# Optimization experiments

Measured on AMD Instinct MI355X. Metric: run time of the kernel, lower is better.

The kernel has to match this reference:

```python
import jax, jax.numpy as jnp
import numpy as np

B, T, N, D_IN, H, K, E, L = 32, 12, 2000, 2, 64, 2, 10, 2


def setup_inputs() -> dict:
    key = jax.random.key(0)
    ks = jax.random.split(key, 2 + 4 * L)
    s = 0.05
    inp = {
        "x": jax.random.normal(ks[0], (B, T, N, D_IN), jnp.float32),
        "node_embeddings": jax.random.normal(ks[1], (N, E), jnp.float32),
    }
    dims_in = [D_IN, H]
    for l in range(L):
        din = dims_in[l] + H  # cell input is concat([x_t, state])
        inp[f"gate_w{l}"] = jax.random.normal(ks[2 + 4 * l], (E, K, din, 2 * H), jnp.float32) * s
        inp[f"gate_b{l}"] = jax.random.normal(ks[3 + 4 * l], (E, 2 * H), jnp.float32) * s
        inp[f"upd_w{l}"] = jax.random.normal(ks[4 + 4 * l], (E, K, din, H), jnp.float32) * s
        inp[f"upd_b{l}"] = jax.random.normal(ks[5 + 4 * l], (E, H), jnp.float32) * s
    return inp


def _supports(node_embeddings):
    # adaptive adjacency from node embeddings + Chebyshev-style link polynomials
    A = jax.nn.softmax(jax.nn.relu(node_embeddings @ node_embeddings.T), axis=1)  # [N,N]
    sup = [jnp.eye(N, dtype=A.dtype), A]
    for _ in range(K - 2):
        sup.append(2.0 * (A @ sup[-1]) - sup[-2])
    return jnp.stack(sup)  # [K,N,N]


def _gconv(x, supports, emb, w_pool, b_pool):
    # x: [B,N,C] -> [B,N,O]; per-node weights generated from embeddings
    W = jnp.einsum('ne,ekio->nkio', emb, w_pool)          # [N,K,C,O]
    b = emb @ b_pool                                       # [N,O]
    xg = jnp.einsum('knm,bmc->bnkc', supports, x)          # graph aggregation
    return jnp.einsum('bnki,nkio->bno', xg, W) + b


def _cell(x_t, h, supports, emb, gw, gb, uw, ub):
    xs = jnp.concatenate([x_t, h], axis=-1)
    zr = jax.nn.sigmoid(_gconv(xs, supports, emb, gw, gb))
    z, r = jnp.split(zr, 2, axis=-1)
    hc = jnp.tanh(_gconv(jnp.concatenate([x_t, z * h], axis=-1), supports, emb, uw, ub))
    return r * h + (1.0 - r) * hc


def reference(x, node_embeddings, gate_w0, gate_b0, upd_w0, upd_b0,
              gate_w1, gate_b1, upd_w1, upd_b1):
    supports = _supports(node_embeddings)
    params = [(gate_w0, gate_b0, upd_w0, upd_b0),
              (gate_w1, gate_b1, upd_w1, upd_b1)]
    cur = x
    last = None
    for gw, gb, uw, ub in params:
        h0 = jnp.zeros((x.shape[0], N, H), x.dtype)

        def step(h, x_t, gw=gw, gb=gb, uw=uw, ub=ub):
            h_new = _cell(x_t, h, supports, node_embeddings, gw, gb, uw, ub)
            return h_new, h_new

        last, outs = jax.lax.scan(step, h0, jnp.swapaxes(cur, 0, 1))
        cur = jnp.swapaxes(outs, 0, 1)  # [B,T,N,H]
    # return_all_layers=False -> last layer's full sequence output and last state
    return cur, last
```

## Files before the change

### kernel.cpp

```cpp
#include <hip/hip_runtime.h>
#include <cstdint>

#define NN 2000
#define NP 2048
#define TT 12
#define BBATCH 32
#define HH 64
#define EE 10

typedef _Float16 f16;
typedef _Float16 f16x8 __attribute__((ext_vector_type(8)));
typedef float f32x4 __attribute__((ext_vector_type(4)));
typedef unsigned int u32;

__device__ __forceinline__ void gld_lds16(const void* g, void* lds) {
    __builtin_amdgcn_global_load_lds(
        (const __attribute__((address_space(1))) u32*)(const void*)g,
        (__attribute__((address_space(3))) u32*)(void*)lds, 16, 0, 0);
}

__global__ __launch_bounds__(256) void k_supports(const float* __restrict__ emb, f16* __restrict__ A2) {
    int n = blockIdx.x;
    int tid = threadIdx.x;
    if (n >= NN) {
        for (int m = tid; m < NP; m += 256) A2[(size_t)n * NP + m] = (f16)0.f;
        return;
    }
    __shared__ float red[4];
    float en[EE];
#pragma unroll
    for (int e = 0; e < EE; e++) en[e] = emb[n * EE + e];
    float g[8];
    float mx = 0.f;
#pragma unroll
    for (int i = 0; i < 8; i++) {
        int m = tid + 256 * i;
        float v = 0.f;
        if (m < NN) {
            float a = 0.f;
#pragma unroll
            for (int e = 0; e < EE; e++) a += en[e] * emb[m * EE + e];
            v = fmaxf(a, 0.f);
            mx = fmaxf(mx, v);
        }
        g[i] = v;
    }
#pragma unroll
    for (int d = 32; d; d >>= 1) mx = fmaxf(mx, __shfl_xor(mx, d));
    if ((tid & 63) == 0) red[tid >> 6] = mx;
    __syncthreads();
    mx = fmaxf(fmaxf(red[0], red[1]), fmaxf(red[2], red[3]));
    float s = 0.f;
#pragma unroll
    for (int i = 0; i < 8; i++) {
        int m = tid + 256 * i;
        if (m < NN) { g[i] = __expf(g[i] - mx); s += g[i]; }
    }
#pragma unroll
    for (int d = 32; d; d >>= 1) s += __shfl_xor(s, d);
    __syncthreads();
    if ((tid & 63) == 0) red[tid >> 6] = s;
    __syncthreads();
    s = red[0] + red[1] + red[2] + red[3];
    float inv = 1.f / s;
#pragma unroll
    for (int i = 0; i < 8; i++) {
        int m = tid + 256 * i;
        A2[(size_t)n * NP + m] = (m < NN) ? (f16)(g[i] * inv) : (f16)0.f;
    }
}

template <int DIN, int O>
__global__ __launch_bounds__(256) void k_wgen(const float* __restrict__ emb,
                                              const float* __restrict__ wpool,
                                              f16* __restrict__ WT) {
    constexpr int DPAD = (DIN == 66) ? 80 : 128;
    constexpr int R = 2 * DPAD;
    int n0 = blockIdx.x * 4;
    int r = threadIdx.x;
    if (r >= R) return;
    int k = (r >= DPAD) ? 1 : 0;
    int c = r - k * DPAD;
    bool valid = (c < DIN);
    float en[4][EE];
#pragma unroll
    for (int j = 0; j < 4; j++)
#pragma unroll
        for (int e = 0; e < EE; e++) en[j][e] = emb[(n0 + j) * EE + e];
    const float* wp = wpool + ((size_t)(k * DIN + (valid ? c : 0))) * O;
    for (int o = 0; o < O; o += 4) {
        float4 a[4] = {};
        if (valid) {
#pragma unroll
            for (int e = 0; e < EE; e++) {
                float4 w4 = *(const float4*)(wp + (size_t)e * 2 * DIN * O + o);
#pragma unroll
                for (int j = 0; j < 4; j++) {
                    a[j].x += en[j][e] * w4.x; a[j].y += en[j][e] * w4.y;
                    a[j].z += en[j][e] * w4.z; a[j].w += en[j][e] * w4.w;
                }
            }
        }
#pragma unroll
        for (int j = 0; j < 4; j++) {
            f16* outp = WT + ((size_t)(n0 + j) * O + o) * R + r;
            outp[0] = (f16)a[j].x; outp[(size_t)R] = (f16)a[j].y;
            outp[(size_t)2 * R] = (f16)a[j].z; outp[(size_t)3 * R] = (f16)a[j].w;
        }
    }
}

__global__ __launch_bounds__(256) void k_xall(const float* __restrict__ x, f16* __restrict__ out) {
    int idx = blockIdx.x * 256 + threadIdx.x;
    if (idx >= 768 * NP) return;
    int r = idx >> 11, n = idx & (NP - 1);
    int t = r >> 6, rb = r & 63, b = rb >> 1, d = rb & 1;
    float v = (n < NN) ? x[(((size_t)b * TT + t) * NN + n) * 2 + d] : 0.f;
    out[idx] = (f16)v;
}

template <int W, int TS, int TO>
__global__ __launch_bounds__(256) void k_tr(const f16* __restrict__ in, f16* __restrict__ out) {
    __shared__ f16 t[64][72];
    int ebx = blockIdx.x * TS + TO, by = blockIdx.y;
    int tid = threadIdx.x;
    int ml = tid >> 2, q = tid & 3;
    int m = by * 64 + ml;
    f16x8 a, b2;
#pragma unroll
    for (int i = 0; i < 8; i++) { a[i] = (f16)0.f; b2[i] = (f16)0.f; }
    if (m < NN) {
        const f16* src = in + (size_t)m * W + ebx * 64 + q * 16;
        a = *(const f16x8*)src;
        b2 = *(const f16x8*)(src + 8);
    }
    *(f16x8*)&t[ml][q * 16] = a;
    *(f16x8*)&t[ml][q * 16 + 8] = b2;
    __syncthreads();
    int jl = tid >> 2;
    f16x8 r0, r1;
#pragma unroll
    for (int i = 0; i < 8; i++) r0[i] = t[q * 16 + i][jl];
#pragma unroll
    for (int i = 0; i < 8; i++) r1[i] = t[q * 16 + 8 + i][jl];
    f16* dst = out + (size_t)(ebx * 64 + jl) * NP + by * 64 + q * 16;
    *(f16x8*)dst = r0;
    *(f16x8*)(dst + 8) = r1;
}

template <int ST, int OFF>
__global__ __launch_bounds__(256) void k_gemm(const f16* __restrict__ A2, const f16* __restrict__ XT,
                                              f16* __restrict__ C, int J) {
    __shared__ __align__(16) f16 at[128 * 64];
    __shared__ __align__(16) f16 xt[64 * 64];
    int tj = blockIdx.x * 64;
    int tm = blockIdx.y * 128;
    int rowbase = (tj >> 6) * ST + OFF;
    int tid = threadIdx.x;
    int w = tid >> 6, l = tid & 63;
    int lr = l & 15, lg = l >> 4;
    f32x4 acc[2][4];
#pragma unroll
    for (int mt = 0; mt < 2; mt++)
#pragma unroll
        for (int nt = 0; nt < 4; nt++) acc[mt][nt] = (f32x4){0.f, 0.f, 0.f, 0.f};

    for (int k0 = 0; k0 < 2048; k0 += 64) {
#pragma unroll
        for (int i = 0; i < 4; i++) {
            int e = w * 2048 + i * 512 + l * 8;
            int row = e >> 6, s = (e >> 3) & 7;
            const f16* src = A2 + (size_t)(tm + row) * 2048 + k0 + ((s ^ (row & 7)) << 3);
            gld_lds16(src, &at[w * 2048 + i * 512]);
        }
#pragma unroll
        for (int i = 0; i < 2; i++) {
            int e = w * 1024 + i * 512 + l * 8;
            int row = e >> 6, s = (e >> 3) & 7;
            const f16* src = XT + (size_t)(rowbase + row) * 2048 + k0 + ((s ^ (row & 7)) << 3);
            gld_lds16(src, &xt[w * 1024 + i * 512]);
        }
        __syncthreads();
#pragma unroll
        for (int kk = 0; kk < 2; kk++) {
            int s = kk * 4 + lg;
            f16x8 av[2], bv[4];
#pragma unroll
            for (int mt = 0; mt < 2; mt++) {
                int row = w * 32 + mt * 16 + lr;
                av[mt] = *(const f16x8*)&at[row * 64 + ((s ^ (row & 7)) << 3)];
            }
#pragma unroll
            for (int nt = 0; nt < 4; nt++) {
                int row = nt * 16 + lr;
                bv[nt] = *(const f16x8*)&xt[row * 64 + ((s ^ (row & 7)) << 3)];
            }
#pragma unroll
            for (int mt = 0; mt < 2; mt++)
#pragma unroll
                for (int nt = 0; nt < 4; nt++)
                    acc[mt][nt] = __builtin_amdgcn_mfma_f32_16x16x32_f16(av[mt], bv[nt], acc[mt][nt], 0, 0, 0);
        }
        __syncthreads();
    }
#pragma unroll
    for (int mt = 0; mt < 2; mt++)
#pragma unroll
        for (int nt = 0; nt < 4; nt++)
#pragma unroll
            for (int q = 0; q < 4; q++) {
                int row = tm + w * 32 + mt * 16 + lg * 4 + q;
                int col = tj + nt * 16 + lr;
                C[(size_t)row * J + col] = (f16)acc[mt][nt][q];
            }
}

__global__ __launch_bounds__(256) void k_gate0(const float* __restrict__ x, int t,
                                               const f16* __restrict__ h0rm, const f16* __restrict__ aggX,
                                               const f16* __restrict__ aggH0, const f16* __restrict__ WT,
                                               const float* __restrict__ bpool, const float* __restrict__ emb,
                                               const float* __restrict__ hbuf,
                                               f16* __restrict__ us_rm, float* __restrict__ rbuf) {
    constexpr int DIN = 66, DPAD = 80, R = 160, RPAD = 168, KCH = 5, O = 128;
    int n = blockIdx.x;
    int tid = threadIdx.x, w = tid >> 6, l = tid & 63;
    int lr = l & 15, lg = l >> 4;
    __shared__ __align__(16) f16 xg[32 * RPAD];

    f16x8 wf[KCH][2];
    const f16* wbase = WT + (size_t)n * O * R;
#pragma unroll
    for (int kk = 0; kk < KCH; kk++)
#pragma unroll
        for (int nt = 0; nt < 2; nt++) {
            int o = w * 32 + nt * 16 + lr;
            wf[kk][nt] = *(const f16x8*)(wbase + (size_t)o * R + kk * 32 + lg * 8);
        }
    for (int i = tid; i < 32 * RPAD / 8; i += 256) *(float4*)&xg[i * 8] = (float4){0.f, 0.f, 0.f, 0.f};
    __syncthreads();
    for (int e = tid; e < 32 * DIN; e += 256) {
        int b = e / DIN, c = e % DIN;
        f16 v1 = (c < 2) ? (f16)x[(((size_t)b * TT + t) * NN + n) * 2 + c]
                         : h0rm[(size_t)n * 2048 + b * 64 + (c - 2)];
        f16 v2 = (c < 2) ? aggX[(size_t)n * 768 + t * 64 + b * 2 + c]
                         : aggH0[(size_t)n * 2048 + b * 64 + (c - 2)];
        xg[b * RPAD + c] = v1;
        xg[b * RPAD + DPAD + c] = v2;
    }
    __syncthreads();

    f32x4 acc[2][2];
#pragma unroll
    for (int mt = 0; mt < 2; mt++)
#pragma unroll
        for (int nt = 0; nt < 2; nt++) acc[mt][nt] = (f32x4){0.f, 0.f, 0.f, 0.f};
#pragma unroll
    for (int kk = 0; kk < KCH; kk++) {
        f16x8 av[2];
#pragma unroll
        for (int mt = 0; mt < 2; mt++)
            av[mt] = *(const f16x8*)&xg[(mt * 16 + lr) * RPAD + kk * 32 + lg * 8];
#pragma unroll
        for (int mt = 0; mt < 2; mt++)
#pragma unroll
            for (int nt = 0; nt < 2; nt++)
                acc[mt][nt] = __builtin_amdgcn_mfma_f32_16x16x32_f16(av[mt], wf[kk][nt], acc[mt][nt], 0, 0, 0);
    }
#pragma unroll
    for (int mt = 0; mt < 2; mt++)
#pragma unroll
        for (int nt = 0; nt < 2; nt++) {
            int o = w * 32 + nt * 16 + lr;
            float bs = 0.f;
#pragma unroll
            for (int e = 0; e < EE; e++) bs += emb[n * EE + e] * bpool[e * 2 * HH + o];
#pragma unroll
            for (int q = 0; q < 4; q++) {
                int b = mt * 16 + lg * 4 + q;
                float v = acc[mt][nt][q] + bs;
                float sg = 1.f / (1.f + __expf(-v));
                if (o < HH) {
                    float u = sg * hbuf[((size_t)n * 32 + b) * HH + o];
                    us_rm[(size_t)n * 2048 + b * 64 + o] = (f16)u;
                } else {
                    rbuf[((size_t)n * 32 + b) * HH + (o - HH)] = sg;
                }
            }
        }
}

__global__ __launch_bounds__(256) void k_upd0(const float* __restrict__ x, int t,
                                              const f16* __restrict__ us0, const f16* __restrict__ aggX,
                                              const f16* __restrict__ uagg, const f16* __restrict__ WT,
                                              const float* __restrict__ bpool, const float* __restrict__ emb,
                                              float* hbuf, const float* __restrict__ rbuf,
                                              f16* __restrict__ h0rm, f16* __restrict__ xs1,
                                              f16* __restrict__ us1) {
    constexpr int DIN = 66, DPAD = 80, R = 160, RPAD = 168, KCH = 5, O = 64;
    int n = blockIdx.x;
    int tid = threadIdx.x, w = tid >> 6, l = tid & 63;
    int lr = l & 15, lg = l >> 4;
    __shared__ __align__(16) f16 xg[32 * RPAD];

    f16x8 wf[KCH];
    const f16* wbase = WT + (size_t)n * O * R;
    int o = w * 16 + lr;
#pragma unroll
    for (int kk = 0; kk < KCH; kk++)
        wf[kk] = *(const f16x8*)(wbase + (size_t)o * R + kk * 32 + lg * 8);

    for (int i = tid; i < 32 * RPAD / 8; i += 256) *(float4*)&xg[i * 8] = (float4){0.f, 0.f, 0.f, 0.f};
    __syncthreads();
    for (int e = tid; e < 32 * DIN; e += 256) {
        int b = e / DIN, c = e % DIN;
        f16 v1 = (c < 2) ? (f16)x[(((size_t)b * TT + t) * NN + n) * 2 + c]
                         : us0[(size_t)n * 2048 + b * 64 + (c - 2)];
        f16 v2 = (c < 2) ? aggX[(size_t)n * 768 + t * 64 + b * 2 + c]
                         : uagg[(size_t)n * 2048 + b * 64 + (c - 2)];
        xg[b * RPAD + c] = v1;
        xg[b * RPAD + DPAD + c] = v2;
    }
    __syncthreads();

    f32x4 acc[2];
    acc[0] = (f32x4){0.f, 0.f, 0.f, 0.f};
    acc[1] = (f32x4){0.f, 0.f, 0.f, 0.f};
#pragma unroll
    for (int kk = 0; kk < KCH; kk++) {
        f16x8 av[2];
#pragma unroll
        for (int mt = 0; mt < 2; mt++)
            av[mt] = *(const f16x8*)&xg[(mt * 16 + lr) * RPAD + kk * 32 + lg * 8];
#pragma unroll
        for (int mt = 0; mt < 2; mt++)
            acc[mt] = __builtin_amdgcn_mfma_f32_16x16x32_f16(av[mt], wf[kk], acc[mt], 0, 0, 0);
    }
    float bias = 0.f;
#pragma unroll
    for (int e = 0; e < EE; e++) bias += emb[n * EE + e] * bpool[e * HH + o];
#pragma unroll
    for (int mt = 0; mt < 2; mt++)
#pragma unroll
        for (int q = 0; q < 4; q++) {
            int b = mt * 16 + lg * 4 + q;
            float v = acc[mt][q] + bias;
            float ex = __expf(2.f * v);
            float hc = 1.f - 2.f / (ex + 1.f);
            size_t hidx = ((size_t)n * 32 + b) * HH + o;
            float r = rbuf[hidx], h = hbuf[hidx];
            float hn = r * h + (1.f - r) * hc;
            hbuf[hidx] = hn;
            f16 hh = (f16)hn;
            h0rm[(size_t)n * 2048 + b * 64 + o] = hh;
            xs1[(size_t)n * 4096 + b * 128 + o] = hh;
            us1[(size_t)n * 4096 + b * 128 + o] = hh;
        }
}

__global__ __launch_bounds__(256) void k_gate1(const f16* __restrict__ xs1,
                                               const f16* __restrict__ aggA, const f16* __restrict__ aggB,
                                               const f16* __restrict__ WT, const float* __restrict__ bpool,
                                               const float* __restrict__ emb, const float* __restrict__ hbuf,
                                               f16* __restrict__ us1, float* __restrict__ rbuf) {
    constexpr int DPAD = 128, R = 256, RPAD = 264, KCH = 8, O = 128;
    int n = blockIdx.x;
    int tid = threadIdx.x, w = tid >> 6, l = tid & 63;
    int lr = l & 15, lg = l >> 4;
    __shared__ __align__(16) f16 xg[32 * RPAD];

    f16x8 wf[KCH][2];
    const f16* wbase = WT + (size_t)n * O * R;
#pragma unroll
    for (int kk = 0; kk < KCH; kk++)
#pragma unroll
        for (int nt = 0; nt < 2; nt++) {
            int o = w * 32 + nt * 16 + lr;
            wf[kk][nt] = *(const f16x8*)(wbase + (size_t)o * R + kk * 32 + lg * 8);
        }
    for (int e8 = tid; e8 < 32 * 16; e8 += 256) {
        int b = e8 >> 4, c8 = e8 & 15;
        *(f16x8*)&xg[b * RPAD + c8 * 8] = *(const f16x8*)&xs1[(size_t)n * 4096 + e8 * 8];
        f16x8 v = (c8 < 8) ? *(const f16x8*)&aggA[(size_t)n * 2048 + b * 64 + c8 * 8]
                           : *(const f16x8*)&aggB[(size_t)n * 2048 + b * 64 + (c8 - 8) * 8];
        *(f16x8*)&xg[b * RPAD + DPAD + c8 * 8] = v;
    }
    __syncthreads();

    f32x4 acc[2][2];
#pragma unroll
    for (int mt = 0; mt < 2; mt++)
#pragma unroll
        for (int nt = 0; nt < 2; nt++) acc[mt][nt] = (f32x4){0.f, 0.f, 0.f, 0.f};
#pragma unroll
    for (int kk = 0; kk < KCH; kk++) {
        f16x8 av[2];
#pragma unroll
        for (int mt = 0; mt < 2; mt++)
            av[mt] = *(const f16x8*)&xg[(mt * 16 + lr) * RPAD + kk * 32 + lg * 8];
#pragma unroll
        for (int mt = 0; mt < 2; mt++)
#pragma unroll
            for (int nt = 0; nt < 2; nt++)
                acc[mt][nt] = __builtin_amdgcn_mfma_f32_16x16x32_f16(av[mt], wf[kk][nt], acc[mt][nt], 0, 0, 0);
    }
#pragma unroll
    for (int mt = 0; mt < 2; mt++)
#pragma unroll
        for (int nt = 0; nt < 2; nt++) {
            int o = w * 32 + nt * 16 + lr;
            float bs = 0.f;
#pragma unroll
            for (int e = 0; e < EE; e++) bs += emb[n * EE + e] * bpool[e * 2 * HH + o];
#pragma unroll
            for (int q = 0; q < 4; q++) {
                int b = mt * 16 + lg * 4 + q;
                float v = acc[mt][nt][q] + bs;
                float sg = 1.f / (1.f + __expf(-v));
                if (o < HH) {
                    float u = sg * hbuf[((size_t)n * 32 + b) * HH + o];
                    us1[(size_t)n * 4096 + b * 128 + 64 + o] = (f16)u;
                } else {
                    rbuf[((size_t)n * 32 + b) * HH + (o - HH)] = sg;
                }
            }
        }
}

__global__ __launch_bounds__(256) void k_upd1(const f16* __restrict__ us1,
                                              const f16* __restrict__ aggA, const f16* __restrict__ aggB,
                                              const f16* __restrict__ WT, const float* __restrict__ bpool,
                                              const float* __restrict__ emb,
                                              float* hbuf, const float* __restrict__ rbuf,
                                              f16* __restrict__ xs1, float* __restrict__ dout, int t) {
    constexpr int DPAD = 128, R = 256, RPAD = 264, KCH = 8, O = 64;
    int n = blockIdx.x;
    int tid = threadIdx.x, w = tid >> 6, l = tid & 63;
    int lr = l & 15, lg = l >> 4;
    __shared__ __align__(16) f16 xg[32 * RPAD];

    f16x8 wf[KCH];
    const f16* wbase = WT + (size_t)n * O * R;
    int o = w * 16 + lr;
#pragma unroll
    for (int kk = 0; kk < KCH; kk++)
        wf[kk] = *(const f16x8*)(wbase + (size_t)o * R + kk * 32 + lg * 8);

    for (int e8 = tid; e8 < 32 * 16; e8 += 256) {
        int b = e8 >> 4, c8 = e8 & 15;
        *(f16x8*)&xg[b * RPAD + c8 * 8] = *(const f16x8*)&us1[(size_t)n * 4096 + e8 * 8];
        f16x8 v = (c8 < 8) ? *(const f16x8*)&aggA[(size_t)n * 2048 + b * 64 + c8 * 8]
                           : *(const f16x8*)&aggB[(size_t)n * 2048 + b * 64 + (c8 - 8) * 8];
        *(f16x8*)&xg[b * RPAD + DPAD + c8 * 8] = v;
    }
    __syncthreads();

    f32x4 acc[2];
    acc[0] = (f32x4){0.f, 0.f, 0.f, 0.f};
    acc[1] = (f32x4){0.f, 0.f, 0.f, 0.f};
#pragma unroll
    for (int kk = 0; kk < KCH; kk++) {
        f16x8 av[2];
#pragma unroll
        for (int mt = 0; mt < 2; mt++)
            av[mt] = *(const f16x8*)&xg[(mt * 16 + lr) * RPAD + kk * 32 + lg * 8];
#pragma unroll
        for (int mt = 0; mt < 2; mt++)
            acc[mt] = __builtin_amdgcn_mfma_f32_16x16x32_f16(av[mt], wf[kk], acc[mt], 0, 0, 0);
    }
    float bias = 0.f;
#pragma unroll
    for (int e = 0; e < EE; e++) bias += emb[n * EE + e] * bpool[e * HH + o];
#pragma unroll
    for (int mt = 0; mt < 2; mt++)
#pragma unroll
        for (int q = 0; q < 4; q++) {
            int b = mt * 16 + lg * 4 + q;
            float v = acc[mt][q] + bias;
            float ex = __expf(2.f * v);
            float hc = 1.f - 2.f / (ex + 1.f);
            size_t hidx = ((size_t)n * 32 + b) * HH + o;
            float r = rbuf[hidx], h = hbuf[hidx];
            float hn = r * h + (1.f - r) * hc;
            hbuf[hidx] = hn;
            f16 hh = (f16)hn;
            xs1[(size_t)n * 4096 + b * 128 + 64 + o] = hh;
            dout[(((size_t)b * TT + t) * NN + n) * HH + o] = hn;
            if (t == TT - 1)
                dout[(size_t)BBATCH * TT * NN * HH + ((size_t)b * NN + n) * HH + o] = hn;
        }
}

extern "C" void kernel_launch(void* const* d_in, const int* in_sizes, int n_in,
                              void* d_out, int out_size, void* d_ws, size_t ws_size,
                              hipStream_t stream) {
    (void)in_sizes; (void)n_in; (void)out_size; (void)ws_size;
    const float* x   = (const float*)d_in[0];
    const float* emb = (const float*)d_in[1];
    const float* gw0 = (const float*)d_in[2];
    const float* gb0 = (const float*)d_in[3];
    const float* uw0 = (const float*)d_in[4];
    const float* ub0 = (const float*)d_in[5];
    const float* gw1 = (const float*)d_in[6];
    const float* gb1 = (const float*)d_in[7];
    const float* uw1 = (const float*)d_in[8];
    const float* ub1 = (const float*)d_in[9];
    float* out = (float*)d_out;

    char* p = (char*)d_ws;
    auto alloc = [&](size_t bytes) { char* r = p; p += (bytes + 255) & ~(size_t)255; return r; };
    f16* A2    = (f16*)alloc((size_t)NP * NP * 2);
    f16* Wg0   = (f16*)alloc((size_t)NN * 128 * 160 * 2);
    f16* Wu0   = (f16*)alloc((size_t)NN * 64 * 160 * 2);
    f16* Wg1   = (f16*)alloc((size_t)NN * 128 * 256 * 2);
    f16* Wu1   = (f16*)alloc((size_t)NN * 64 * 256 * 2);
    f16* xTall = (f16*)alloc((size_t)768 * NP * 2);
    f16* aggX  = (f16*)alloc((size_t)NP * 768 * 2);
    f16* h0rm  = (f16*)alloc((size_t)NN * 2048 * 2);
    f16* us0   = (f16*)alloc((size_t)NN * 2048 * 2);
    f16* usT0  = (f16*)alloc((size_t)2048 * NP * 2);
    f16* uagg0 = (f16*)alloc((size_t)NP * 2048 * 2);
    f16* aggH0 = (f16*)alloc((size_t)NP * 2048 * 2);
    f16* aggH1 = (f16*)alloc((size_t)NP * 2048 * 2);
    f16* xs1   = (f16*)alloc((size_t)NN * 4096 * 2);
    f16* xsT1  = (f16*)alloc((size_t)4096 * NP * 2);
    f16* us1   = (f16*)alloc((size_t)NN * 4096 * 2);
    f16* usT1  = (f16*)alloc((size_t)4096 * NP * 2);
    f16* uagg1 = (f16*)alloc((size_t)NP * 2048 * 2);
    float* h0  = (float*)alloc((size_t)NN * 32 * 64 * 4);
    float* r0  = (float*)alloc((size_t)NN * 32 * 64 * 4);
    float* h1  = (float*)alloc((size_t)NN * 32 * 64 * 4);
    float* r1  = (float*)alloc((size_t)NN * 32 * 64 * 4);

    hipMemsetAsync(h0rm, 0, (size_t)NN * 2048 * 2, stream);
    hipMemsetAsync(xs1, 0, (size_t)NN * 4096 * 2, stream);
    hipMemsetAsync(aggH0, 0, (size_t)NP * 2048 * 2, stream);
    hipMemsetAsync(aggH1, 0, (size_t)NP * 2048 * 2, stream);
    hipMemsetAsync(h0, 0, (size_t)NN * 32 * 64 * 4, stream);
    hipMemsetAsync(h1, 0, (size_t)NN * 32 * 64 * 4, stream);

    k_supports<<<NP, 256, 0, stream>>>(emb, A2);
    k_wgen<66, 128><<<NN / 4, 256, 0, stream>>>(emb, gw0, Wg0);
    k_wgen<66, 64><<<NN / 4, 256, 0, stream>>>(emb, uw0, Wu0);
    k_wgen<128, 128><<<NN / 4, 256, 0, stream>>>(emb, gw1, Wg1);
    k_wgen<128, 64><<<NN / 4, 256, 0, stream>>>(emb, uw1, Wu1);
    k_xall<<<768 * NP / 256, 256, 0, stream>>>(x, xTall);
    k_gemm<64, 0><<<dim3(12, 16), 256, 0, stream>>>(A2, xTall, aggX, 768);

    for (int t = 0; t < TT; t++) {
        k_gate0<<<NN, 256, 0, stream>>>(x, t, h0rm, aggX, aggH0, Wg0, gb0, emb, h0, us0, r0);
        k_tr<2048, 1, 0><<<dim3(32, 32), 256, 0, stream>>>(us0, usT0);
        k_gemm<64, 0><<<dim3(32, 16), 256, 0, stream>>>(A2, usT0, uagg0, 2048);
        k_upd0<<<NN, 256, 0, stream>>>(x, t, us0, aggX, uagg0, Wu0, ub0, emb, h0, r0,
                                       h0rm, xs1, us1);
        k_tr<4096, 2, 0><<<dim3(32, 32), 256, 0, stream>>>(xs1, xsT1);
        k_gemm<128, 0><<<dim3(32, 16), 256, 0, stream>>>(A2, xsT1, aggH0, 2048);
        k_gate1<<<NN, 256, 0, stream>>>(xs1, aggH0, aggH1, Wg1, gb1, emb, h1, us1, r1);
        k_tr<4096, 2, 1><<<dim3(32, 32), 256, 0, stream>>>(us1, usT1);
        k_gemm<128, 64><<<dim3(32, 16), 256, 0, stream>>>(A2, usT1, uagg1, 2048);
        k_upd1<<<NN, 256, 0, stream>>>(us1, aggH0, uagg1, Wu1, ub1, emb, h1, r1,
                                       xs1, out, t);
        k_tr<4096, 2, 1><<<dim3(32, 32), 256, 0, stream>>>(xs1, xsT1);
        k_gemm<128, 64><<<dim3(32, 16), 256, 0, stream>>>(A2, xsT1, aggH1, 2048);
    }
}
```

Measured before the change: 4.036 ms.

## Merge layer-0/layer-1 hidden aggregations into one GEMM and split-K the update GEMMs

Aggregates the full xs1 buffer (h0 and h1 halves) in a single wider GEMM once per step, replacing two separate transpose+GEMM passes, so aggH0 and aggH1 share one interleaved buffer. The update-gate aggregation GEMMs, which only launch 512 blocks, become a split-K kernel over a z-dimension of 2 writing fp32 partials. The upd kernels then sum the partials while loading. This removes a transpose and a GEMM per step and raises GPU occupancy for the small GEMMs, at the cost of extra fp32 partial traffic.

```diff
diff --git a/kernel.cpp b/kernel.cpp
--- a/kernel.cpp
+++ b/kernel.cpp
@@ -215,13 +215,81 @@
             }
 }
 
+template <int ST, int OFF>
+__global__ __launch_bounds__(256) void k_gemmk2(const f16* __restrict__ A2, const f16* __restrict__ XT,
+                                                float* __restrict__ P) {
+    __shared__ __align__(16) f16 at[128 * 64];
+    __shared__ __align__(16) f16 xt[64 * 64];
+    int tj = blockIdx.x * 64;
+    int tm = blockIdx.y * 128;
+    int kz = blockIdx.z;
+    int rowbase = (tj >> 6) * ST + OFF;
+    int tid = threadIdx.x;
+    int w = tid >> 6, l = tid & 63;
+    int lr = l & 15, lg = l >> 4;
+    f32x4 acc[2][4];
+#pragma unroll
+    for (int mt = 0; mt < 2; mt++)
+#pragma unroll
+        for (int nt = 0; nt < 4; nt++) acc[mt][nt] = (f32x4){0.f, 0.f, 0.f, 0.f};
+
+    for (int k0 = kz * 1024; k0 < kz * 1024 + 1024; k0 += 64) {
+#pragma unroll
+        for (int i = 0; i < 4; i++) {
+            int e = w * 2048 + i * 512 + l * 8;
+            int row = e >> 6, s = (e >> 3) & 7;
+            const f16* src = A2 + (size_t)(tm + row) * 2048 + k0 + ((s ^ (row & 7)) << 3);
+            gld_lds16(src, &at[w * 2048 + i * 512]);
+        }
+#pragma unroll
+        for (int i = 0; i < 2; i++) {
+            int e = w * 1024 + i * 512 + l * 8;
+            int row = e >> 6, s = (e >> 3) & 7;
+            const f16* src = XT + (size_t)(rowbase + row) * 2048 + k0 + ((s ^ (row & 7)) << 3);
+            gld_lds16(src, &xt[w * 1024 + i * 512]);
+        }
+        __syncthreads();
+#pragma unroll
+        for (int kk = 0; kk < 2; kk++) {
+            int s = kk * 4 + lg;
+            f16x8 av[2], bv[4];
+#pragma unroll
+            for (int mt = 0; mt < 2; mt++) {
+                int row = w * 32 + mt * 16 + lr;
+                av[mt] = *(const f16x8*)&at[row * 64 + ((s ^ (row & 7)) << 3)];
+            }
+#pragma unroll
+            for (int nt = 0; nt < 4; nt++) {
+                int row = nt * 16 + lr;
+                bv[nt] = *(const f16x8*)&xt[row * 64 + ((s ^ (row & 7)) << 3)];
+            }
+#pragma unroll
+            for (int mt = 0; mt < 2; mt++)
+#pragma unroll
+                for (int nt = 0; nt < 4; nt++)
+                    acc[mt][nt] = __builtin_amdgcn_mfma_f32_16x16x32_f16(av[mt], bv[nt], acc[mt][nt], 0, 0, 0);
+        }
+        __syncthreads();
+    }
+#pragma unroll
+    for (int mt = 0; mt < 2; mt++)
+#pragma unroll
+        for (int nt = 0; nt < 4; nt++)
+#pragma unroll
+            for (int q = 0; q < 4; q++) {
+                int row = tm + w * 32 + mt * 16 + lg * 4 + q;
+                int col = tj + nt * 16 + lr;
+                P[((size_t)kz * 2048 + row) * 2048 + col] = acc[mt][nt][q];
+            }
+}
+
 __global__ __launch_bounds__(256) void k_gate0(const float* __restrict__ x, int t,
                                                const f16* __restrict__ h0rm, const f16* __restrict__ aggX,
-                                               const f16* __restrict__ aggH0, const f16* __restrict__ WT,
+                                               const f16* __restrict__ aggH01, const f16* __restrict__ WT,
                                                const float* __restrict__ bpool, const float* __restrict__ emb,
                                                const float* __restrict__ hbuf,
                                                f16* __restrict__ us_rm, float* __restrict__ rbuf) {
-    constexpr int DIN = 66, DPAD = 80, R = 160, RPAD = 168, KCH = 5, O = 128;
+    constexpr int DIN = 66, DPAD = 80, RPAD = 168, KCH = 5, O = 128, R = 160;
     int n = blockIdx.x;
     int tid = threadIdx.x, w = tid >> 6, l = tid & 63;
     int lr = l & 15, lg = l >> 4;
@@ -243,7 +311,7 @@
         f16 v1 = (c < 2) ? (f16)x[(((size_t)b * TT + t) * NN + n) * 2 + c]
                          : h0rm[(size_t)n * 2048 + b * 64 + (c - 2)];
         f16 v2 = (c < 2) ? aggX[(size_t)n * 768 + t * 64 + b * 2 + c]
-                         : aggH0[(size_t)n * 2048 + b * 64 + (c - 2)];
+                         : aggH01[(size_t)n * 4096 + b * 128 + (c - 2)];
         xg[b * RPAD + c] = v1;
         xg[b * RPAD + DPAD + c] = v2;
     }
@@ -291,12 +359,12 @@
 
 __global__ __launch_bounds__(256) void k_upd0(const float* __restrict__ x, int t,
                                               const f16* __restrict__ us0, const f16* __restrict__ aggX,
-                                              const f16* __restrict__ uagg, const f16* __restrict__ WT,
+                                              const float* __restrict__ P, const f16* __restrict__ WT,
                                               const float* __restrict__ bpool, const float* __restrict__ emb,
                                               float* hbuf, const float* __restrict__ rbuf,
                                               f16* __restrict__ h0rm, f16* __restrict__ xs1,
                                               f16* __restrict__ us1) {
-    constexpr int DIN = 66, DPAD = 80, R = 160, RPAD = 168, KCH = 5, O = 64;
+    constexpr int DIN = 66, DPAD = 80, RPAD = 168, KCH = 5, O = 64, R = 160;
     int n = blockIdx.x;
     int tid = threadIdx.x, w = tid >> 6, l = tid & 63;
     int lr = l & 15, lg = l >> 4;
@@ -315,8 +383,13 @@
         int b = e / DIN, c = e % DIN;
         f16 v1 = (c < 2) ? (f16)x[(((size_t)b * TT + t) * NN + n) * 2 + c]
                          : us0[(size_t)n * 2048 + b * 64 + (c - 2)];
-        f16 v2 = (c < 2) ? aggX[(size_t)n * 768 + t * 64 + b * 2 + c]
-                         : uagg[(size_t)n * 2048 + b * 64 + (c - 2)];
+        f16 v2;
+        if (c < 2) {
+            v2 = aggX[(size_t)n * 768 + t * 64 + b * 2 + c];
+        } else {
+            size_t idx = (size_t)n * 2048 + b * 64 + (c - 2);
+            v2 = (f16)(P[idx] + P[(size_t)2048 * 2048 + idx]);
+        }
         xg[b * RPAD + c] = v1;
         xg[b * RPAD + DPAD + c] = v2;
     }
@@ -358,11 +431,11 @@
 }
 
 __global__ __launch_bounds__(256) void k_gate1(const f16* __restrict__ xs1,
-                                               const f16* __restrict__ aggA, const f16* __restrict__ aggB,
+                                               const f16* __restrict__ aggH01,
                                                const f16* __restrict__ WT, const float* __restrict__ bpool,
                                                const float* __restrict__ emb, const float* __restrict__ hbuf,
                                                f16* __restrict__ us1, float* __restrict__ rbuf) {
-    constexpr int DPAD = 128, R = 256, RPAD = 264, KCH = 8, O = 128;
+    constexpr int DPAD = 128, RPAD = 264, KCH = 8, O = 128, R = 256;
     int n = blockIdx.x;
     int tid = threadIdx.x, w = tid >> 6, l = tid & 63;
     int lr = l & 15, lg = l >> 4;
@@ -380,9 +453,7 @@
     for (int e8 = tid; e8 < 32 * 16; e8 += 256) {
         int b = e8 >> 4, c8 = e8 & 15;
         *(f16x8*)&xg[b * RPAD + c8 * 8] = *(const f16x8*)&xs1[(size_t)n * 4096 + e8 * 8];
-        f16x8 v = (c8 < 8) ? *(const f16x8*)&aggA[(size_t)n * 2048 + b * 64 + c8 * 8]
-                           : *(const f16x8*)&aggB[(size_t)n * 2048 + b * 64 + (c8 - 8) * 8];
-        *(f16x8*)&xg[b * RPAD + DPAD + c8 * 8] = v;
+        *(f16x8*)&xg[b * RPAD + DPAD + c8 * 8] = *(const f16x8*)&aggH01[(size_t)n * 4096 + e8 * 8];
     }
     __syncthreads();
 
@@ -427,12 +498,12 @@
 }
 
 __global__ __launch_bounds__(256) void k_upd1(const f16* __restrict__ us1,
-                                              const f16* __restrict__ aggA, const f16* __restrict__ aggB,
+                                              const f16* __restrict__ aggH01, const float* __restrict__ P,
                                               const f16* __restrict__ WT, const float* __restrict__ bpool,
                                               const float* __restrict__ emb,
                                               float* hbuf, const float* __restrict__ rbuf,
                                               f16* __restrict__ xs1, float* __restrict__ dout, int t) {
-    constexpr int DPAD = 128, R = 256, RPAD = 264, KCH = 8, O = 64;
+    constexpr int DPAD = 128, RPAD = 264, KCH = 8, O = 64, R = 256;
     int n = blockIdx.x;
     int tid = threadIdx.x, w = tid >> 6, l = tid & 63;
     int lr = l & 15, lg = l >> 4;
@@ -448,8 +519,20 @@
     for (int e8 = tid; e8 < 32 * 16; e8 += 256) {
         int b = e8 >> 4, c8 = e8 & 15;
         *(f16x8*)&xg[b * RPAD + c8 * 8] = *(const f16x8*)&us1[(size_t)n * 4096 + e8 * 8];
-        f16x8 v = (c8 < 8) ? *(const f16x8*)&aggA[(size_t)n * 2048 + b * 64 + c8 * 8]
-                           : *(const f16x8*)&aggB[(size_t)n * 2048 + b * 64 + (c8 - 8) * 8];
+        f16x8 v;
+        if (c8 < 8) {
+            v = *(const f16x8*)&aggH01[(size_t)n * 4096 + b * 128 + c8 * 8];
+        } else {
+            size_t idx = (size_t)n * 2048 + b * 64 + (c8 - 8) * 8;
+            float4 a0 = *(const float4*)&P[idx];
+            float4 a1 = *(const float4*)&P[idx + 4];
+            float4 b0 = *(const float4*)&P[(size_t)2048 * 2048 + idx];
+            float4 b1 = *(const float4*)&P[(size_t)2048 * 2048 + idx + 4];
+            v[0] = (f16)(a0.x + b0.x); v[1] = (f16)(a0.y + b0.y);
+            v[2] = (f16)(a0.z + b0.z); v[3] = (f16)(a0.w + b0.w);
+            v[4] = (f16)(a1.x + b1.x); v[5] = (f16)(a1.y + b1.y);
+            v[6] = (f16)(a1.z + b1.z); v[7] = (f16)(a1.w + b1.w);
+        }
         *(f16x8*)&xg[b * RPAD + DPAD + c8 * 8] = v;
     }
     __syncthreads();
@@ -508,33 +591,30 @@
 
     char* p = (char*)d_ws;
     auto alloc = [&](size_t bytes) { char* r = p; p += (bytes + 255) & ~(size_t)255; return r; };
-    f16* A2    = (f16*)alloc((size_t)NP * NP * 2);
-    f16* Wg0   = (f16*)alloc((size_t)NN * 128 * 160 * 2);
-    f16* Wu0   = (f16*)alloc((size_t)NN * 64 * 160 * 2);
-    f16* Wg1   = (f16*)alloc((size_t)NN * 128 * 256 * 2);
-    f16* Wu1   = (f16*)alloc((size_t)NN * 64 * 256 * 2);
-    f16* xTall = (f16*)alloc((size_t)768 * NP * 2);
-    f16* aggX  = (f16*)alloc((size_t)NP * 768 * 2);
-    f16* h0rm  = (f16*)alloc((size_t)NN * 2048 * 2);
-    f16* us0   = (f16*)alloc((size_t)NN * 2048 * 2);
-    f16* usT0  = (f16*)alloc((size_t)2048 * NP * 2);
-    f16* uagg0 = (f16*)alloc((size_t)NP * 2048 * 2);
-    f16* aggH0 = (f16*)alloc((size_t)NP * 2048 * 2);
-    f16* aggH1 = (f16*)alloc((size_t)NP * 2048 * 2);
-    f16* xs1   = (f16*)alloc((size_t)NN * 4096 * 2);
-    f16* xsT1  = (f16*)alloc((size_t)4096 * NP * 2);
-    f16* us1   = (f16*)alloc((size_t)NN * 4096 * 2);
-    f16* usT1  = (f16*)alloc((size_t)4096 * NP * 2);
-    f16* uagg1 = (f16*)alloc((size_t)NP * 2048 * 2);
-    float* h0  = (float*)alloc((size_t)NN * 32 * 64 * 4);
-    float* r0  = (float*)alloc((size_t)NN * 32 * 64 * 4);
-    float* h1  = (float*)alloc((size_t)NN * 32 * 64 * 4);
-    float* r1  = (float*)alloc((size_t)NN * 32 * 64 * 4);
+    f16* A2     = (f16*)alloc((size_t)NP * NP * 2);
+    f16* Wg0    = (f16*)alloc((size_t)NN * 128 * 160 * 2);
+    f16* Wu0    = (f16*)alloc((size_t)NN * 64 * 160 * 2);
+    f16* Wg1    = (f16*)alloc((size_t)NN * 128 * 256 * 2);
+    f16* Wu1    = (f16*)alloc((size_t)NN * 64 * 256 * 2);
+    f16* xTall  = (f16*)alloc((size_t)768 * NP * 2);
+    f16* aggX   = (f16*)alloc((size_t)NP * 768 * 2);
+    f16* h0rm   = (f16*)alloc((size_t)NN * 2048 * 2);
+    f16* us0    = (f16*)alloc((size_t)NN * 2048 * 2);
+    f16* usT0   = (f16*)alloc((size_t)2048 * NP * 2);
+    float* Pbuf = (float*)alloc((size_t)2 * 2048 * 2048 * 4);
+    f16* aggH01 = (f16*)alloc((size_t)NP * 4096 * 2);
+    f16* xs1    = (f16*)alloc((size_t)NN * 4096 * 2);
+    f16* xsT1   = (f16*)alloc((size_t)4096 * NP * 2);
+    f16* us1    = (f16*)alloc((size_t)NN * 4096 * 2);
+    f16* usT1   = (f16*)alloc((size_t)4096 * NP * 2);
+    float* h0   = (float*)alloc((size_t)NN * 32 * 64 * 4);
+    float* r0   = (float*)alloc((size_t)NN * 32 * 64 * 4);
+    float* h1   = (float*)alloc((size_t)NN * 32 * 64 * 4);
+    float* r1   = (float*)alloc((size_t)NN * 32 * 64 * 4);
 
     hipMemsetAsync(h0rm, 0, (size_t)NN * 2048 * 2, stream);
     hipMemsetAsync(xs1, 0, (size_t)NN * 4096 * 2, stream);
-    hipMemsetAsync(aggH0, 0, (size_t)NP * 2048 * 2, stream);
-    hipMemsetAsync(aggH1, 0, (size_t)NP * 2048 * 2, stream);
+    hipMemsetAsync(aggH01, 0, (size_t)NP * 4096 * 2, stream);
     hipMemsetAsync(h0, 0, (size_t)NN * 32 * 64 * 4, stream);
     hipMemsetAsync(h1, 0, (size_t)NN * 32 * 64 * 4, stream);
 
@@ -547,19 +627,17 @@
     k_gemm<64, 0><<<dim3(12, 16), 256, 0, stream>>>(A2, xTall, aggX, 768);
 
     for (int t = 0; t < TT; t++) {
-        k_gate0<<<NN, 256, 0, stream>>>(x, t, h0rm, aggX, aggH0, Wg0, gb0, emb, h0, us0, r0);
+        k_gate0<<<NN, 256, 0, stream>>>(x, t, h0rm, aggX, aggH01, Wg0, gb0, emb, h0, us0, r0);
         k_tr<2048, 1, 0><<<dim3(32, 32), 256, 0, stream>>>(us0, usT0);
-        k_gemm<64, 0><<<dim3(32, 16), 256, 0, stream>>>(A2, usT0, uagg0, 2048);
-        k_upd0<<<NN, 256, 0, stream>>>(x, t, us0, aggX, uagg0, Wu0, ub0, emb, h0, r0,
+        k_gemmk2<64, 0><<<dim3(32, 16, 2), 256, 0, stream>>>(A2, usT0, Pbuf);
+        k_upd0<<<NN, 256, 0, stream>>>(x, t, us0, aggX, Pbuf, Wu0, ub0, emb, h0, r0,
                                        h0rm, xs1, us1);
-        k_tr<4096, 2, 0><<<dim3(32, 32), 256, 0, stream>>>(xs1, xsT1);
-        k_gemm<128, 0><<<dim3(32, 16), 256, 0, stream>>>(A2, xsT1, aggH0, 2048);
-        k_gate1<<<NN, 256, 0, stream>>>(xs1, aggH0, aggH1, Wg1, gb1, emb, h1, us1, r1);
+        k_tr<4096, 1, 0><<<dim3(64, 32), 256, 0, stream>>>(xs1, xsT1);
+        k_gemm<64, 0><<<dim3(64, 16), 256, 0, stream>>>(A2, xsT1, aggH01, 4096);
+        k_gate1<<<NN, 256, 0, stream>>>(xs1, aggH01, Wg1, gb1, emb, h1, us1, r1);
         k_tr<4096, 2, 1><<<dim3(32, 32), 256, 0, stream>>>(us1, usT1);
-        k_gemm<128, 64><<<dim3(32, 16), 256, 0, stream>>>(A2, usT1, uagg1, 2048);
-        k_upd1<<<NN, 256, 0, stream>>>(us1, aggH0, uagg1, Wu1, ub1, emb, h1, r1,
+        k_gemmk2<128, 64><<<dim3(32, 16, 2), 256, 0, stream>>>(A2, usT1, Pbuf);
+        k_upd1<<<NN, 256, 0, stream>>>(us1, aggH01, Pbuf, Wu1, ub1, emb, h1, r1,
                                        xs1, out, t);
-        k_tr<4096, 2, 1><<<dim3(32, 32), 256, 0, stream>>>(xs1, xsT1);
-        k_gemm<128, 64><<<dim3(32, 16), 256, 0, stream>>>(A2, xsT1, aggH1, 2048);
-    }
-}
+    }
+}
```

After: 3.904 ms. 3.3% less time.
